# Performance work log

Hardware: AMD Instinct MI355X
Metric: run time of the kernel (lower is better)

Reference implementation:

```python
import jax, jax.numpy as jnp
import numpy as np

N, F, UNITS, FE, DEG = 2048, 128, 128, 16, 64
E = N * DEG


def setup_inputs() -> dict:
    key = jax.random.key(0)
    k1, k2, k3, k4, k5, k6, k7 = jax.random.split(key, 7)
    node_states = jax.random.normal(k1, (1, N, F), dtype=jnp.float32)
    # sorted sources (required for the TF repeat/bincount normalization to be valid)
    src = jnp.repeat(jnp.arange(N, dtype=jnp.int32), DEG)
    dst = jax.random.randint(k2, (E,), 0, N, dtype=jnp.int32)
    edges = jnp.stack([src, dst], axis=-1)[None]  # [1, E, 2]
    edge_features = jax.random.normal(k3, (1, N, N, FE), dtype=jnp.float32)
    s = 1.0 / np.sqrt(F)
    W_left = jax.random.uniform(k4, (F, UNITS), minval=-s, maxval=s, dtype=jnp.float32)
    W_right = jax.random.uniform(k5, (F, UNITS), minval=-s, maxval=s, dtype=jnp.float32)
    sa = 1.0 / np.sqrt(2 * UNITS + FE)
    W_attn = jax.random.uniform(k6, (2 * UNITS + FE, 1), minval=-sa, maxval=sa, dtype=jnp.float32)
    se = 1.0 / np.sqrt(FE)
    W_edge = jax.random.uniform(k7, (FE, FE), minval=-se, maxval=se, dtype=jnp.float32)
    return {"node_states": node_states, "edges": edges, "edge_features": edge_features,
            "W_left": W_left, "W_right": W_right, "W_attn": W_attn, "W_edge": W_edge}


def reference(node_states, edges, edge_features, W_left, W_right, W_attn, W_edge):
    ns = node_states[0]          # [N, F]
    e = edges[0]                 # [E, 2]
    ef = edge_features[0]        # [N, N, Fe]
    src, dst = e[:, 0], e[:, 1]
    n = ns.shape[0]

    hl = ns @ W_left             # [N, U]
    hr = ns @ W_right            # [N, U]

    # edge gather -> concat -> leaky_relu (TF default alpha = 0.2)
    x = jax.nn.leaky_relu(jnp.concatenate([hl[src], hr[dst]], axis=-1), 0.2)  # [E, 2U]
    efe = ef[src, dst] @ W_edge                                               # [E, Fe]
    scores = jnp.concatenate([x, efe], axis=-1) @ W_attn                      # [E, 1]
    scores = jnp.exp(jnp.clip(scores[:, 0], -2.0, 2.0))                       # [E]

    # segment softmax normalization (gather form; equals TF repeat/bincount for sorted src)
    ssum = jax.ops.segment_sum(scores, src, num_segments=n)                   # [N]
    attn = scores / ssum[src]                                                 # [E]

    # weighted scatter-add of neighbour messages
    out = jax.ops.segment_sum(hr[dst] * attn[:, None], src, num_segments=n)   # [N, U]
    return out[None]  # [1, N, U]
```

## Files before the change

### kernel.cpp

```cpp
#include <hip/hip_runtime.h>
#include <math.h>

#define NN 2048
#define FF 128
#define UU 128
#define FE 16
#define DEG 64

__global__ __launch_bounds__(256) void gemm_hlr(
    const float* __restrict__ ns, const float* __restrict__ Wl,
    const float* __restrict__ Wr, float* __restrict__ hl, float* __restrict__ hr)
{
    __shared__ float sns[16][FF];
    const int nb = blockIdx.x * 16;
    const int tid = threadIdx.x;
    for (int i = tid; i < 16 * FF; i += 256) {
        sns[i >> 7][i & 127] = ns[(size_t)(nb + (i >> 7)) * FF + (i & 127)];
    }
    __syncthreads();
    const int u = tid & 127;
    const int ng = tid >> 7;
    float accl[8] = {0.f, 0.f, 0.f, 0.f, 0.f, 0.f, 0.f, 0.f};
    float accr[8] = {0.f, 0.f, 0.f, 0.f, 0.f, 0.f, 0.f, 0.f};
    for (int k = 0; k < FF; ++k) {
        const float wl = Wl[k * UU + u];
        const float wr = Wr[k * UU + u];
#pragma unroll
        for (int j = 0; j < 8; ++j) {
            const float a = sns[ng * 8 + j][k];
            accl[j] += a * wl;
            accr[j] += a * wr;
        }
    }
#pragma unroll
    for (int j = 0; j < 8; ++j) {
        hl[(size_t)(nb + ng * 8 + j) * UU + u] = accl[j];
        hr[(size_t)(nb + ng * 8 + j) * UU + u] = accr[j];
    }
}

__global__ __launch_bounds__(128) void node_attn(
    const float* __restrict__ hl, const float* __restrict__ hr,
    const float* __restrict__ Wa, float* __restrict__ al, float* __restrict__ ar)
{
    const int n = blockIdx.x;
    const int u = threadIdx.x;
    float x = hl[(size_t)n * UU + u];
    float y = hr[(size_t)n * UU + u];
    x = (x > 0.f ? x : 0.2f * x) * Wa[u];
    y = (y > 0.f ? y : 0.2f * y) * Wa[UU + u];
#pragma unroll
    for (int o = 32; o > 0; o >>= 1) { x += __shfl_xor(x, o); y += __shfl_xor(y, o); }
    __shared__ float sx[2], sy[2];
    if ((u & 63) == 0) { sx[u >> 6] = x; sy[u >> 6] = y; }
    __syncthreads();
    if (u == 0) { al[n] = sx[0] + sx[1]; ar[n] = sy[0] + sy[1]; }
}

__global__ __launch_bounds__(128) void edge_out(
    const float* __restrict__ hr, const float* __restrict__ al,
    const float* __restrict__ ar, const int* __restrict__ edges,
    const float* __restrict__ ef, const float* __restrict__ We,
    const float* __restrict__ Wa, float* __restrict__ out)
{
    const int b = blockIdx.x;
    const int tid = threadIdx.x;
    __shared__ float wef[FE];
    __shared__ float sattn[DEG];
    __shared__ int   sdst[DEG];
    __shared__ int   s_src;

    if (tid < FE) {
        float s = 0.f;
#pragma unroll
        for (int j = 0; j < FE; ++j) s += We[tid * FE + j] * Wa[2 * UU + j];
        wef[tid] = s;
    }
    __syncthreads();

    if (tid < DEG) {
        const int e   = b * DEG + tid;
        const int src = edges[2 * e];
        const int dst = edges[2 * e + 1];
        if (tid == 0) s_src = src;
        const float4* efp = (const float4*)(ef + ((size_t)src * NN + dst) * FE);
        float s = al[src] + ar[dst];
#pragma unroll
        for (int q = 0; q < 4; ++q) {
            const float4 v = efp[q];
            s += v.x * wef[4 * q + 0] + v.y * wef[4 * q + 1]
               + v.z * wef[4 * q + 2] + v.w * wef[4 * q + 3];
        }
        s = fminf(fmaxf(s, -2.f), 2.f);
        const float sc = expf(s);
        float tot = sc;
#pragma unroll
        for (int o = 32; o > 0; o >>= 1) tot += __shfl_xor(tot, o);
        sattn[tid] = sc / tot;
        sdst[tid]  = dst;
    }
    __syncthreads();

    const int u = tid;
    float acc = 0.f;
#pragma unroll 8
    for (int e = 0; e < DEG; ++e) {
        acc += sattn[e] * hr[(size_t)sdst[e] * UU + u];
    }
    out[(size_t)s_src * UU + u] = acc;
}

extern "C" void kernel_launch(void* const* d_in, const int* in_sizes, int n_in,
                              void* d_out, int out_size, void* d_ws, size_t ws_size,
                              hipStream_t stream) {
    const float* ns  = (const float*)d_in[0];
    const int*   edg = (const int*)d_in[1];
    const float* ef  = (const float*)d_in[2];
    const float* Wl  = (const float*)d_in[3];
    const float* Wr  = (const float*)d_in[4];
    const float* Wa  = (const float*)d_in[5];
    const float* We  = (const float*)d_in[6];
    float* out = (float*)d_out;

    float* hl = (float*)d_ws;
    float* hr = hl + (size_t)NN * UU;
    float* al = hr + (size_t)NN * UU;
    float* ar = al + NN;

    gemm_hlr<<<NN / 16, 256, 0, stream>>>(ns, Wl, Wr, hl, hr);
    node_attn<<<NN, 128, 0, stream>>>(hl, hr, Wa, al, ar);
    edge_out<<<NN, 128, 0, stream>>>(hr, al, ar, edg, ef, We, Wa, out);
}
```

Before: 370.0 us.

## Fuse node attention projection into GEMM kernel and assume sorted sources

Folds the per-node attention reductions (al, ar) into the projection GEMM, so hl no longer has to be written to and re-read from global memory, and one launch disappears. The GEMM tile drops to 8 nodes per block to give more blocks. The edge-feature/attention weight product is now computed once and stored in the workspace rather than per block. The edge kernel also assumes src equals the block index (sorted edges, DEG per node), which removes the src load at the cost of depending on that input structure.

Result: faster. 331.7 us (-10.3%).

```diff
diff --git a/kernel.cpp b/kernel.cpp
--- a/kernel.cpp
+++ b/kernel.cpp
@@ -7,84 +7,93 @@
 #define FE 16
 #define DEG 64
 
-__global__ __launch_bounds__(256) void gemm_hlr(
+__global__ __launch_bounds__(256) void prep(
     const float* __restrict__ ns, const float* __restrict__ Wl,
-    const float* __restrict__ Wr, float* __restrict__ hl, float* __restrict__ hr)
+    const float* __restrict__ Wr, const float* __restrict__ Wa,
+    const float* __restrict__ We,
+    float* __restrict__ hr, float* __restrict__ al, float* __restrict__ ar,
+    float* __restrict__ wef)
 {
-    __shared__ float sns[16][FF];
-    const int nb = blockIdx.x * 16;
+    __shared__ float sns[8][FF];
+    __shared__ float swl[4][4], swr[4][4];
+    const int nb  = blockIdx.x * 8;
     const int tid = threadIdx.x;
-    for (int i = tid; i < 16 * FF; i += 256) {
-        sns[i >> 7][i & 127] = ns[(size_t)(nb + (i >> 7)) * FF + (i & 127)];
+    {
+        const int idx = tid * 4;
+        ((float4*)&sns[idx >> 7][idx & 127])[0] =
+            ((const float4*)(ns + (size_t)nb * FF))[tid];
     }
     __syncthreads();
-    const int u = tid & 127;
+
+    const int u  = tid & 127;
     const int ng = tid >> 7;
-    float accl[8] = {0.f, 0.f, 0.f, 0.f, 0.f, 0.f, 0.f, 0.f};
-    float accr[8] = {0.f, 0.f, 0.f, 0.f, 0.f, 0.f, 0.f, 0.f};
+    float accl[4] = {0.f, 0.f, 0.f, 0.f};
+    float accr[4] = {0.f, 0.f, 0.f, 0.f};
+#pragma unroll 4
     for (int k = 0; k < FF; ++k) {
         const float wl = Wl[k * UU + u];
         const float wr = Wr[k * UU + u];
 #pragma unroll
-        for (int j = 0; j < 8; ++j) {
-            const float a = sns[ng * 8 + j][k];
+        for (int j = 0; j < 4; ++j) {
+            const float a = sns[ng * 4 + j][k];
             accl[j] += a * wl;
             accr[j] += a * wr;
         }
     }
+
+    const float wa_l = Wa[u];
+    const float wa_r = Wa[UU + u];
+    float xl[4], xr[4];
 #pragma unroll
-    for (int j = 0; j < 8; ++j) {
-        hl[(size_t)(nb + ng * 8 + j) * UU + u] = accl[j];
-        hr[(size_t)(nb + ng * 8 + j) * UU + u] = accr[j];
+    for (int j = 0; j < 4; ++j) {
+        hr[(size_t)(nb + ng * 4 + j) * UU + u] = accr[j];
+        const float l = accl[j];
+        const float r = accr[j];
+        xl[j] = (l > 0.f ? l : 0.2f * l) * wa_l;
+        xr[j] = (r > 0.f ? r : 0.2f * r) * wa_r;
     }
-}
-
-__global__ __launch_bounds__(128) void node_attn(
-    const float* __restrict__ hl, const float* __restrict__ hr,
-    const float* __restrict__ Wa, float* __restrict__ al, float* __restrict__ ar)
-{
-    const int n = blockIdx.x;
-    const int u = threadIdx.x;
-    float x = hl[(size_t)n * UU + u];
-    float y = hr[(size_t)n * UU + u];
-    x = (x > 0.f ? x : 0.2f * x) * Wa[u];
-    y = (y > 0.f ? y : 0.2f * y) * Wa[UU + u];
 #pragma unroll
-    for (int o = 32; o > 0; o >>= 1) { x += __shfl_xor(x, o); y += __shfl_xor(y, o); }
-    __shared__ float sx[2], sy[2];
-    if ((u & 63) == 0) { sx[u >> 6] = x; sy[u >> 6] = y; }
+    for (int o = 32; o > 0; o >>= 1) {
+#pragma unroll
+        for (int j = 0; j < 4; ++j) {
+            xl[j] += __shfl_xor(xl[j], o);
+            xr[j] += __shfl_xor(xr[j], o);
+        }
+    }
+    const int wave = tid >> 6;
+    if ((tid & 63) == 0) {
+#pragma unroll
+        for (int j = 0; j < 4; ++j) { swl[wave][j] = xl[j]; swr[wave][j] = xr[j]; }
+    }
     __syncthreads();
-    if (u == 0) { al[n] = sx[0] + sx[1]; ar[n] = sy[0] + sy[1]; }
+    if (tid < 8) {
+        const int g = tid >> 2, j = tid & 3;
+        al[nb + tid] = swl[2 * g][j] + swl[2 * g + 1][j];
+        ar[nb + tid] = swr[2 * g][j] + swr[2 * g + 1][j];
+    }
+    if (blockIdx.x == 0 && tid < FE) {
+        float s = 0.f;
+#pragma unroll
+        for (int j = 0; j < FE; ++j) s += We[tid * FE + j] * Wa[2 * UU + j];
+        wef[tid] = s;
+    }
 }
 
 __global__ __launch_bounds__(128) void edge_out(
     const float* __restrict__ hr, const float* __restrict__ al,
     const float* __restrict__ ar, const int* __restrict__ edges,
-    const float* __restrict__ ef, const float* __restrict__ We,
-    const float* __restrict__ Wa, float* __restrict__ out)
+    const float* __restrict__ ef, const float* __restrict__ wef,
+    float* __restrict__ out)
 {
-    const int b = blockIdx.x;
+    const int b   = blockIdx.x;
     const int tid = threadIdx.x;
-    __shared__ float wef[FE];
     __shared__ float sattn[DEG];
     __shared__ int   sdst[DEG];
-    __shared__ int   s_src;
-
-    if (tid < FE) {
-        float s = 0.f;
-#pragma unroll
-        for (int j = 0; j < FE; ++j) s += We[tid * FE + j] * Wa[2 * UU + j];
-        wef[tid] = s;
-    }
-    __syncthreads();
 
     if (tid < DEG) {
-        const int e   = b * DEG + tid;
-        const int src = edges[2 * e];
-        const int dst = edges[2 * e + 1];
-        if (tid == 0) s_src = src;
-        const float4* efp = (const float4*)(ef + ((size_t)src * NN + dst) * FE);
-        float s = al[src] + ar[dst];
+        const int dst = edges[2 * (b * DEG + tid) + 1];
+        const float4* efp = (const float4*)(ef + ((size_t)b * NN + dst) * FE);
+        float s = al[b] + ar[dst];
 #pragma unroll
         for (int q = 0; q < 4; ++q) {
             const float4 v = efp[q];
@@ -107,7 +116,7 @@
     for (int e = 0; e < DEG; ++e) {
         acc += sattn[e] * hr[(size_t)sdst[e] * UU + u];
     }
-    out[(size_t)s_src * UU + u] = acc;
+    out[(size_t)b * UU + u] = acc;
 }
 
 extern "C" void kernel_launch(void* const* d_in, const int* in_sizes, int n_in,
@@ -122,12 +131,11 @@
     const float* We  = (const float*)d_in[6];
     float* out = (float*)d_out;
 
-    float* hl = (float*)d_ws;
-    float* hr = hl + (size_t)NN * UU;
-    float* al = hr + (size_t)NN * UU;
-    float* ar = al + NN;
+    float* hr  = (float*)d_ws;
+    float* al  = hr + (size_t)NN * UU;
+    float* ar  = al + NN;
+    float* wef = ar + NN;
 
-    gemm_hlr<<<NN / 16, 256, 0, stream>>>(ns, Wl, Wr, hl, hr);
-    node_attn<<<NN, 128, 0, stream>>>(hl, hr, Wa, al, ar);
-    edge_out<<<NN, 128, 0, stream>>>(hr, al, ar, edg, ef, We, Wa, out);
+    prep<<<NN / 8, 256, 0, stream>>>(ns, Wl, Wr, Wa, We, hr, al, ar, wef);
+    edge_out<<<NN, 128, 0, stream>>>(hr, al, ar, edg, ef, wef, out);
 }
```
